# Kernel optimization log

Hardware: AMD Instinct MI355X
Metric: run time of the kernel (lower is better)

The kernel has to match this reference:

```python
import jax, jax.numpy as jnp
import numpy as np

N, IN_DIM, OUT_DIM, HEADS = 8192, 256, 128, 2


def setup_inputs() -> dict:
    key = jax.random.key(0)
    k1, k2, k3, k4, k5 = jax.random.split(key, 5)
    features = jax.random.normal(k1, (N, IN_DIM), dtype=jnp.float32)
    adjacency = jax.random.randint(k2, (N, N), 0, 2, dtype=jnp.int32)
    # nn.Linear(input_dim, output_dim*heads, bias=False): weight [out, in]
    W = jax.random.normal(k3, (OUT_DIM * HEADS, IN_DIM), dtype=jnp.float32) * 0.05
    attn_src = jax.random.normal(k4, (HEADS, OUT_DIM), dtype=jnp.float32) * 0.05
    attn_dst = jax.random.normal(k5, (HEADS, OUT_DIM), dtype=jnp.float32) * 0.05
    return {"features": features, "adjacency": adjacency, "W": W,
            "attn_src": attn_src, "attn_dst": attn_dst}


def reference(features, adjacency, W, attn_src, attn_dst):
    n = features.shape[0]
    # transformed: [N, H, F]
    transformed = (features @ W.T).reshape(n, HEADS, OUT_DIM)
    src_scores = jnp.einsum('nhf,hf->nh', transformed, attn_src)  # [N, H]
    dst_scores = jnp.einsum('nhf,hf->nh', transformed, attn_dst)  # [N, H]
    # logits: [N_src, N_dst, H]
    logits = jax.nn.leaky_relu(src_scores[:, None, :] + dst_scores[None, :, :],
                               negative_slope=0.2)
    mask = adjacency > 0  # [N, N]
    logits = jnp.where(mask[:, :, None], logits, -jnp.inf)
    attention = jax.nn.softmax(logits, axis=1)  # softmax over dst dim (dim=1)
    attention = jnp.nan_to_num(attention, nan=0.0, posinf=0.0, neginf=0.0)
    aggregated = jnp.einsum('ijh,jhf->ihf', attention, transformed)  # [N, H, F]
    return aggregated.mean(axis=1)  # [N, F]
```

## Files before the change

kernel.cpp:

```cpp
#include <hip/hip_runtime.h>
#include <stdint.h>
#include <stddef.h>

#define NN 8192
#define KD 256
#define CD 256
#define FD 128
#define BI 128
#define BJ 64
#define LOG2E 1.44269504f

typedef __attribute__((ext_vector_type(4))) float f32x4;
typedef __attribute__((ext_vector_type(2))) float f32x2;
typedef __attribute__((ext_vector_type(8))) short b16x8;

__device__ __forceinline__ unsigned int cvtpk(float lo, float hi) {
    unsigned int r;
    asm("v_cvt_pk_bf16_f32 %0, %1, %2" : "=v"(r) : "v"(lo), "v"(hi));
    return r;
}

__device__ __forceinline__ float exp2raw(float x) {
    float r;
    asm("v_exp_f32 %0, %1\n\ts_nop 0" : "=v"(r) : "v"(x));
    return r;
}

__device__ __forceinline__ void async16(const void* g, void* l) {
    __builtin_amdgcn_global_load_lds(
        (const __attribute__((address_space(1))) unsigned int*)g,
        (__attribute__((address_space(3))) unsigned int*)l, 16, 0, 0);
}

__global__ __launch_bounds__(256) void k_transform(
    const float* __restrict__ feat, const float* __restrict__ W,
    const float* __restrict__ asrc, const float* __restrict__ adst,
    unsigned short* __restrict__ Tt, float* __restrict__ s, float* __restrict__ d)
{
    __shared__ unsigned short a_lds[32 * 32];
    __shared__ unsigned short b_lds[256 * 32];
    __shared__ unsigned short tr_lds[256 * 40];
    __shared__ float sc_lds[4][32];
    __shared__ float dc_lds[4][32];

    const int t = threadIdx.x;
    const int wave = t >> 6, lane = t & 63;
    const int l15 = lane & 15, quad = lane >> 4;
    const int n0 = blockIdx.x * 32;

    f32x4 acc[2][4] = {};
    for (int kc = 0; kc < 8; ++kc) {
        const int k0 = kc * 32;
        __syncthreads();
        if (t < 128) {
            const int ai = t >> 2, ag = t & 3;
            const float* src = feat + (size_t)(n0 + ai) * KD + k0 + ag * 8;
            const float4 v0 = *(const float4*)src;
            const float4 v1 = *(const float4*)(src + 4);
            union { unsigned int u[4]; b16x8 v; } pk;
            pk.u[0] = cvtpk(v0.x, v0.y); pk.u[1] = cvtpk(v0.z, v0.w);
            pk.u[2] = cvtpk(v1.x, v1.y); pk.u[3] = cvtpk(v1.z, v1.w);
            const int slot = ag ^ ((ai >> 1) & 3);
            *(b16x8*)&a_lds[ai * 32 + slot * 8] = pk.v;
        }
        for (int p = 0; p < 4; ++p) {
            const int G = p * 256 + t;
            const int c = G >> 2, g = G & 3;
            const float* src = W + (size_t)c * KD + k0 + g * 8;
            const float4 v0 = *(const float4*)src;
            const float4 v1 = *(const float4*)(src + 4);
            union { unsigned int u[4]; b16x8 v; } pk;
            pk.u[0] = cvtpk(v0.x, v0.y); pk.u[1] = cvtpk(v0.z, v0.w);
            pk.u[2] = cvtpk(v1.x, v1.y); pk.u[3] = cvtpk(v1.z, v1.w);
            const int slot = g ^ ((c >> 1) & 3);
            *(b16x8*)&b_lds[c * 32 + slot * 8] = pk.v;
        }
        __syncthreads();
        b16x8 af[2], bfr[4];
        for (int mt = 0; mt < 2; ++mt) {
            const int m = mt * 16 + l15;
            af[mt] = *(const b16x8*)&a_lds[m * 32 + (quad ^ ((m >> 1) & 3)) * 8];
        }
        for (int nt = 0; nt < 4; ++nt) {
            const int c = wave * 64 + nt * 16 + l15;
            bfr[nt] = *(const b16x8*)&b_lds[c * 32 + (quad ^ ((c >> 1) & 3)) * 8];
        }
        for (int mt = 0; mt < 2; ++mt)
            for (int nt = 0; nt < 4; ++nt)
                acc[mt][nt] = __builtin_amdgcn_mfma_f32_16x16x32_bf16(
                    af[mt], bfr[nt], acc[mt][nt], 0, 0, 0);
    }

    float aS[4], aD[4];
    for (int nt = 0; nt < 4; ++nt) {
        const int c = wave * 64 + nt * 16 + l15;
        aS[nt] = asrc[c]; aD[nt] = adst[c];
    }
    for (int mt = 0; mt < 2; ++mt)
        for (int r = 0; r < 4; ++r) {
            float vs = 0.f, vd = 0.f;
            for (int nt = 0; nt < 4; ++nt) {
                const float x = acc[mt][nt][r];
                vs += x * aS[nt]; vd += x * aD[nt];
            }
            vs += __shfl_xor(vs, 1); vd += __shfl_xor(vd, 1);
            vs += __shfl_xor(vs, 2); vd += __shfl_xor(vd, 2);
            vs += __shfl_xor(vs, 4); vd += __shfl_xor(vd, 4);
            vs += __shfl_xor(vs, 8); vd += __shfl_xor(vd, 8);
            if (l15 == 0) {
                const int nl = mt * 16 + quad * 4 + r;
                sc_lds[wave][nl] = vs; dc_lds[wave][nl] = vd;
            }
        }
    for (int mt = 0; mt < 2; ++mt)
        for (int nt = 0; nt < 4; ++nt) {
            const int c = wave * 64 + nt * 16 + l15;
            const int n = mt * 16 + quad * 4;
            *(unsigned int*)&tr_lds[c * 40 + n] =
                cvtpk(acc[mt][nt][0], acc[mt][nt][1]);
            *(unsigned int*)&tr_lds[c * 40 + n + 2] =
                cvtpk(acc[mt][nt][2], acc[mt][nt][3]);
        }
    __syncthreads();
    if (t < 64) {
        const int n = t >> 1, h = t & 1;
        s[(size_t)(n0 + n) * 2 + h] = (sc_lds[h * 2][n] + sc_lds[h * 2 + 1][n]) * LOG2E;
        d[(size_t)(n0 + n) * 2 + h] = (dc_lds[h * 2][n] + dc_lds[h * 2 + 1][n]) * LOG2E;
    }
    for (int p = 0; p < 4; ++p) {
        const int idx = p * 256 + t;
        const int c = idx >> 2, g = idx & 3;
        *(b16x8*)(Tt + (size_t)c * NN + n0 + g * 8) = *(const b16x8*)&tr_lds[c * 40 + g * 8];
    }
}

__global__ __launch_bounds__(1024, 4) void k_gat(
    const int* __restrict__ adj, const unsigned short* __restrict__ Tt,
    const float* __restrict__ s, const float* __restrict__ d,
    float* __restrict__ num_part,
    float* __restrict__ den_part,
    int jchunk)
{
    __shared__ unsigned short tt_lds[2][CD * BJ];
    __shared__ unsigned short w_lds[2 * BI * BJ];

    const int t = threadIdx.x;
    const int w = t >> 6, lane = t & 63;
    const int l15 = lane & 15, quad = lane >> 4;
    const int rh = w & 3;
    const int cq = w >> 2;
    const int h  = cq >> 1;
    const int fh = cq & 1;
    const int i0 = blockIdx.x * BI;
    const int chunk = blockIdx.y;
    const int jbase = chunk * jchunk;

    const int wi = t >> 3;
    const int j8 = t & 7;
    const int gi = i0 + wi;
    const f32x2 s01 = *(const f32x2*)(s + (size_t)gi * 2);
    const int cbase = h * 128 + fh * 64;

    f32x4 acc[2][4] = {};
    float den0 = 0.f, den1 = 0.f;
    const int njt = jchunk / BJ;

    const int* arow = adj + (size_t)gi * NN + j8 * 8;
    const float* drow = d + (size_t)j8 * 16;
    const int c0 = w * 8 + (lane >> 3);
    const int g0 = (lane & 7) ^ (c0 & 7);
    const unsigned short* tsrc0 = Tt + (size_t)c0 * NN + g0 * 8;
    const int toff0 = w * 1024;
    const int slot = (j8 ^ (wi & 7)) << 3;
    unsigned short* wp0 = &w_lds[(0 * BI + wi) * BJ + slot];
    const int m0 = rh * 32 + l15;
    const int afb = (h * BI + m0) * BJ;
    const int bfb = (cbase + l15) * BJ;
    const int X[2] = {((0 * 4 + quad) ^ (l15 & 7)) << 3,
                      ((1 * 4 + quad) ^ (l15 & 7)) << 3};

    #pragma unroll
    for (int p = 0; p < 2; ++p)
        async16(tsrc0 + (size_t)p * 128 * NN + jbase,
                (char*)&tt_lds[0][0] + toff0 + p * 16384);
    int4 aA0 = *(const int4*)(arow + jbase);
    int4 aA1 = *(const int4*)(arow + jbase + 4);
    const float4* dpp = (const float4*)(drow + 2 * jbase);
    float4 dA0 = dpp[0], dA1 = dpp[1], dA2 = dpp[2], dA3 = dpp[3];
    int4 aB0, aB1; float4 dB0, dB1, dB2, dB3;

    auto body = [&](int jt, int buf,
                    int4& ca0, int4& ca1, float4& cd0, float4& cd1, float4& cd2, float4& cd3,
                    int4& na0, int4& na1, float4& nd0, float4& nd1, float4& nd2, float4& nd3) {
        const int j0 = jbase + jt * BJ;
        __builtin_amdgcn_s_barrier();
        const int jn = (jt + 1 < njt) ? j0 + BJ : j0;
        #pragma unroll
        for (int p = 0; p < 2; ++p)
            async16(tsrc0 + (size_t)p * 128 * NN + jn,
                    (char*)&tt_lds[buf ^ 1][0] + toff0 + p * 16384);
        na0 = *(const int4*)(arow + jn);
        na1 = *(const int4*)(arow + jn + 4);
        { const float4* dnp = (const float4*)(drow + 2 * jn);
          nd0 = dnp[0]; nd1 = dnp[1]; nd2 = dnp[2]; nd3 = dnp[3]; }
        union { float4 v[4]; f32x2 p[8]; } dv;
        dv.v[0] = cd0; dv.v[1] = cd1; dv.v[2] = cd2; dv.v[3] = cd3;
        const int am[8] = {ca0.x, ca0.y, ca0.z, ca0.w, ca1.x, ca1.y, ca1.z, ca1.w};
        f32x2 ef[8];
        f32x2 dp = {0.f, 0.f};
        #pragma unroll
        for (int e = 0; e < 8; ++e) {
            const f32x2 x = s01 + dv.p[e];
            const f32x2 xm = __builtin_elementwise_max(x, 0.2f * x);
            const float r0 = exp2raw(xm.x), r1 = exp2raw(xm.y);
            const f32x2 em = {am[e] != 0 ? r0 : 0.f, am[e] != 0 ? r1 : 0.f};
            ef[e] = em; dp += em;
        }
        den0 += dp.x; den1 += dp.y;
        union { unsigned int u[4]; b16x8 v; } w0, w1;
        #pragma unroll
        for (int q = 0; q < 4; ++q) {
            w0.u[q] = cvtpk(ef[2 * q].x, ef[2 * q + 1].x);
            w1.u[q] = cvtpk(ef[2 * q].y, ef[2 * q + 1].y);
        }
        *(b16x8*)wp0 = w0.v;
        *(b16x8*)(wp0 + BI * BJ) = w1.v;
        asm volatile("s_waitcnt vmcnt(8) lgkmcnt(0)" ::: "memory");
        __builtin_amdgcn_s_barrier();
        __builtin_amdgcn_sched_barrier(0);
        __builtin_amdgcn_s_setprio(1);
        #pragma unroll
        for (int ks = 0; ks < 2; ++ks) {
            b16x8 af[2], bf[4];
            #pragma unroll
            for (int mt = 0; mt < 2; ++mt)
                af[mt] = *(const b16x8*)&w_lds[afb + mt * 1024 + X[ks]];
            #pragma unroll
            for (int nt = 0; nt < 4; ++nt)
                bf[nt] = *(const b16x8*)&tt_lds[buf][bfb + nt * 1024 + X[ks]];
            #pragma unroll
            for (int mt = 0; mt < 2; ++mt)
                #pragma unroll
                for (int nt = 0; nt < 4; ++nt)
                    acc[mt][nt] = __builtin_amdgcn_mfma_f32_16x16x32_bf16(
                        af[mt], bf[nt], acc[mt][nt], 0, 0, 0);
        }
        __builtin_amdgcn_s_setprio(0);
    };

    for (int jt = 0; jt < njt; jt += 2) {
        body(jt,     0, aA0, aA1, dA0, dA1, dA2, dA3, aB0, aB1, dB0, dB1, dB2, dB3);
        body(jt + 1, 1, aB0, aB1, dB0, dB1, dB2, dB3, aA0, aA1, dA0, dA1, dA2, dA3);
    }
    asm volatile("s_waitcnt vmcnt(0)" ::: "memory");
    den0 += __shfl_xor(den0, 1); den0 += __shfl_xor(den0, 2); den0 += __shfl_xor(den0, 4);
    den1 += __shfl_xor(den1, 1); den1 += __shfl_xor(den1, 2); den1 += __shfl_xor(den1, 4);
    if (j8 == 0) {
        den_part[((size_t)chunk * 2 + 0) * NN + gi] = den0;
        den_part[((size_t)chunk * 2 + 1) * NN + gi] = den1;
    }
    float* np_ = num_part + (size_t)chunk * NN * CD;
    for (int mt = 0; mt < 2; ++mt)
        for (int nt = 0; nt < 4; ++nt)
            for (int r = 0; r < 4; ++r) {
                const int n = i0 + rh * 32 + mt * 16 + quad * 4 + r;
                const int c = cbase + nt * 16 + l15;
                np_[(size_t)n * CD + c] = acc[mt][nt][r];
            }
}

__global__ __launch_bounds__(256) void k_combine(
    const float* __restrict__ num_part, const float* __restrict__ den_part,
    float* __restrict__ out, int jsplit)
{
    const int idx = blockIdx.x * 256 + threadIdx.x;
    const int n = idx >> 7, f = idx & 127;
    const size_t row = (size_t)n * CD;
    float n0 = 0.f, n1 = 0.f, d0 = 0.f, d1 = 0.f;
    for (int c = 0; c < jsplit; ++c) {
        const size_t base = (size_t)c * NN * CD;
        n0 += num_part[base + row + f];
        n1 += num_part[base + row + 128 + f];
        d0 += den_part[((size_t)c * 2 + 0) * NN + n];
        d1 += den_part[((size_t)c * 2 + 1) * NN + n];
    }
    const float r0 = d0 != 0.f ? n0 / d0 : 0.f;
    const float r1 = d1 != 0.f ? n1 / d1 : 0.f;
    out[idx] = 0.5f * (r0 + r1);
}

extern "C" void kernel_launch(void* const* d_in, const int* in_sizes, int n_in,
                              void* d_out, int out_size, void* d_ws, size_t ws_size,
                              hipStream_t stream) {
    const float* feat = (const float*)d_in[0];
    const int*   adj  = (const int*)d_in[1];
    const float* W    = (const float*)d_in[2];
    const float* asrc = (const float*)d_in[3];
    const float* adst = (const float*)d_in[4];
    float* out = (float*)d_out;

    const int jsplit = (ws_size >= ((size_t)40 << 20)) ? 4 : 2;
    const int jchunk = NN / jsplit;

    char* ws = (char*)d_ws;
    unsigned short* Tt = (unsigned short*)ws;
    float* s    = (float*)(ws + ((size_t)4 << 20));
    float* dsc  = (float*)(ws + ((size_t)4 << 20) + (64 << 10));
    float* den  = (float*)(ws + ((size_t)4 << 20) + (128 << 10));
    float* nump = (float*)(ws + ((size_t)8 << 20));

    k_transform<<<256, 256, 0, stream>>>(feat, W, asrc, adst, Tt, s, dsc);
    k_gat<<<dim3(NN / BI, jsplit), 1024, 0, stream>>>(adj, Tt, s, dsc, nump, den, jchunk);
    k_combine<<<NN * FD / 256, 256, 0, stream>>>(nump, den, out, jsplit);
}
```

Before: 425.6 us.

## Pack adjacency into bitmask in transform kernel and compute weights in MFMA registers

Extra blocks in the fused transform kernel pack the int32 adjacency matrix into 64-bit ballot bitmasks. The attention kernel then reads bits instead of full ints and builds the exp weights directly in the MFMA A-operand registers, dropping the w_lds staging buffer and its LDS round trip. Each wave now covers 16 rows by 128 columns for one head, and jsplit grows to 4 or 8 depending on workspace size. The adjacency is still read once, but the bitmask pass is an added step, and the larger jsplit means more partial sums to write and combine.

```diff
diff --git a/kernel.cpp b/kernel.cpp
--- a/kernel.cpp
+++ b/kernel.cpp
@@ -32,10 +32,12 @@
         (__attribute__((address_space(3))) unsigned int*)l, 16, 0, 0);
 }
 
-__global__ __launch_bounds__(256) void k_transform(
+__global__ __launch_bounds__(256) void k_fused(
     const float* __restrict__ feat, const float* __restrict__ W,
     const float* __restrict__ asrc, const float* __restrict__ adst,
-    unsigned short* __restrict__ Tt, float* __restrict__ s, float* __restrict__ d)
+    const int* __restrict__ adj,
+    unsigned short* __restrict__ Tt, float* __restrict__ s, float* __restrict__ d,
+    unsigned long long* __restrict__ bits)
 {
     __shared__ unsigned short a_lds[32 * 32];
     __shared__ unsigned short b_lds[256 * 32];
@@ -44,6 +46,19 @@
     __shared__ float dc_lds[4][32];
 
     const int t = threadIdx.x;
+    if (blockIdx.x >= 256) {
+        const int lane = t & 63;
+        const int gw = (blockIdx.x - 256) * 4 + (t >> 6);
+        const int nwaves = (gridDim.x - 256) * 4;
+        const int total = NN * (NN / 64);
+        for (int idx = gw; idx < total; idx += nwaves) {
+            const int row = idx >> 7, w64 = idx & 127;
+            const int v = adj[(size_t)row * NN + w64 * 64 + lane];
+            const unsigned long long m = __ballot(v != 0);
+            if (lane == 0) bits[idx] = m;
+        }
+        return;
+    }
     const int wave = t >> 6, lane = t & 63;
     const int l15 = lane & 15, quad = lane >> 4;
     const int n0 = blockIdx.x * 32;
@@ -124,8 +139,8 @@
     __syncthreads();
     if (t < 64) {
         const int n = t >> 1, h = t & 1;
-        s[(size_t)(n0 + n) * 2 + h] = (sc_lds[h * 2][n] + sc_lds[h * 2 + 1][n]) * LOG2E;
-        d[(size_t)(n0 + n) * 2 + h] = (dc_lds[h * 2][n] + dc_lds[h * 2 + 1][n]) * LOG2E;
+        s[(size_t)h * NN + n0 + n] = (sc_lds[h * 2][n] + sc_lds[h * 2 + 1][n]) * LOG2E;
+        d[(size_t)h * NN + n0 + n] = (dc_lds[h * 2][n] + dc_lds[h * 2 + 1][n]) * LOG2E;
     }
     for (int p = 0; p < 4; ++p) {
         const int idx = p * 256 + t;
@@ -134,48 +149,38 @@
     }
 }
 
-__global__ __launch_bounds__(1024, 4) void k_gat(
-    const int* __restrict__ adj, const unsigned short* __restrict__ Tt,
+__global__ __launch_bounds__(1024, 8) void k_gat(
+    const unsigned long long* __restrict__ bits, const unsigned short* __restrict__ Tt,
     const float* __restrict__ s, const float* __restrict__ d,
     float* __restrict__ num_part,
     float* __restrict__ den_part,
     int jchunk)
 {
     __shared__ unsigned short tt_lds[2][CD * BJ];
-    __shared__ unsigned short w_lds[2 * BI * BJ];
 
     const int t = threadIdx.x;
     const int w = t >> 6, lane = t & 63;
     const int l15 = lane & 15, quad = lane >> 4;
-    const int rh = w & 3;
-    const int cq = w >> 2;
-    const int h  = cq >> 1;
-    const int fh = cq & 1;
+    const int rh = w & 7;
+    const int h  = w >> 3;
     const int i0 = blockIdx.x * BI;
     const int chunk = blockIdx.y;
     const int jbase = chunk * jchunk;
-
-    const int wi = t >> 3;
-    const int j8 = t & 7;
-    const int gi = i0 + wi;
-    const f32x2 s01 = *(const f32x2*)(s + (size_t)gi * 2);
-    const int cbase = h * 128 + fh * 64;
-
-    f32x4 acc[2][4] = {};
-    float den0 = 0.f, den1 = 0.f;
+    const int irow = i0 + rh * 16 + l15;
+    const float sr = s[(size_t)h * NN + irow];
     const int njt = jchunk / BJ;
 
-    const int* arow = adj + (size_t)gi * NN + j8 * 8;
-    const float* drow = d + (size_t)j8 * 16;
+    f32x4 acc[8] = {};
+    float den = 0.f;
+
     const int c0 = w * 8 + (lane >> 3);
     const int g0 = (lane & 7) ^ (c0 & 7);
     const unsigned short* tsrc0 = Tt + (size_t)c0 * NN + g0 * 8;
     const int toff0 = w * 1024;
-    const int slot = (j8 ^ (wi & 7)) << 3;
-    unsigned short* wp0 = &w_lds[(0 * BI + wi) * BJ + slot];
-    const int m0 = rh * 32 + l15;
-    const int afb = (h * BI + m0) * BJ;
-    const int bfb = (cbase + l15) * BJ;
+    const unsigned long long* brow = bits + (size_t)irow * (NN >> 6);
+    const int wb = jbase >> 6;
+    const float* drow = d + (size_t)h * NN + quad * 8;
+    const int bfb = (h * 128 + l15) * BJ;
     const int X[2] = {((0 * 4 + quad) ^ (l15 & 7)) << 3,
                       ((1 * 4 + quad) ^ (l15 & 7)) << 3};
 
@@ -183,90 +188,77 @@
     for (int p = 0; p < 2; ++p)
         async16(tsrc0 + (size_t)p * 128 * NN + jbase,
                 (char*)&tt_lds[0][0] + toff0 + p * 16384);
-    int4 aA0 = *(const int4*)(arow + jbase);
-    int4 aA1 = *(const int4*)(arow + jbase + 4);
-    const float4* dpp = (const float4*)(drow + 2 * jbase);
-    float4 dA0 = dpp[0], dA1 = dpp[1], dA2 = dpp[2], dA3 = dpp[3];
-    int4 aB0, aB1; float4 dB0, dB1, dB2, dB3;
-
-    auto body = [&](int jt, int buf,
-                    int4& ca0, int4& ca1, float4& cd0, float4& cd1, float4& cd2, float4& cd3,
-                    int4& na0, int4& na1, float4& nd0, float4& nd1, float4& nd2, float4& nd3) {
+
+    int buf = 0;
+    for (int jt = 0; jt < njt; ++jt) {
         const int j0 = jbase + jt * BJ;
         __builtin_amdgcn_s_barrier();
+        const unsigned long long cb = brow[wb + jt];
+        const float4 dv0 = *(const float4*)(drow + j0);
+        const float4 dv1 = *(const float4*)(drow + j0 + 4);
+        const float4 dv2 = *(const float4*)(drow + j0 + 32);
+        const float4 dv3 = *(const float4*)(drow + j0 + 36);
         const int jn = (jt + 1 < njt) ? j0 + BJ : j0;
         #pragma unroll
         for (int p = 0; p < 2; ++p)
             async16(tsrc0 + (size_t)p * 128 * NN + jn,
                     (char*)&tt_lds[buf ^ 1][0] + toff0 + p * 16384);
-        na0 = *(const int4*)(arow + jn);
-        na1 = *(const int4*)(arow + jn + 4);
-        { const float4* dnp = (const float4*)(drow + 2 * jn);
-          nd0 = dnp[0]; nd1 = dnp[1]; nd2 = dnp[2]; nd3 = dnp[3]; }
-        union { float4 v[4]; f32x2 p[8]; } dv;
-        dv.v[0] = cd0; dv.v[1] = cd1; dv.v[2] = cd2; dv.v[3] = cd3;
-        const int am[8] = {ca0.x, ca0.y, ca0.z, ca0.w, ca1.x, ca1.y, ca1.z, ca1.w};
-        f32x2 ef[8];
-        f32x2 dp = {0.f, 0.f};
-        #pragma unroll
-        for (int e = 0; e < 8; ++e) {
-            const f32x2 x = s01 + dv.p[e];
-            const f32x2 xm = __builtin_elementwise_max(x, 0.2f * x);
-            const float r0 = exp2raw(xm.x), r1 = exp2raw(xm.y);
-            const f32x2 em = {am[e] != 0 ? r0 : 0.f, am[e] != 0 ? r1 : 0.f};
-            ef[e] = em; dp += em;
-        }
-        den0 += dp.x; den1 += dp.y;
-        union { unsigned int u[4]; b16x8 v; } w0, w1;
-        #pragma unroll
-        for (int q = 0; q < 4; ++q) {
-            w0.u[q] = cvtpk(ef[2 * q].x, ef[2 * q + 1].x);
-            w1.u[q] = cvtpk(ef[2 * q].y, ef[2 * q + 1].y);
-        }
-        *(b16x8*)wp0 = w0.v;
-        *(b16x8*)(wp0 + BI * BJ) = w1.v;
-        asm volatile("s_waitcnt vmcnt(8) lgkmcnt(0)" ::: "memory");
+        const unsigned int by0 = (unsigned int)(cb >> (quad * 8)) & 0xffu;
+        const unsigned int by1 = (unsigned int)(cb >> (32 + quad * 8)) & 0xffu;
+        union { unsigned int u[4]; b16x8 v; } pa0, pa1;
+        {
+            const float dj[8] = {dv0.x, dv0.y, dv0.z, dv0.w, dv1.x, dv1.y, dv1.z, dv1.w};
+            float ef[8];
+            #pragma unroll
+            for (int e = 0; e < 8; ++e) {
+                float x = sr + dj[e]; x = fmaxf(x, 0.2f * x);
+                ef[e] = ((by0 >> e) & 1u) ? exp2raw(x) : 0.f;
+                den += ef[e];
+            }
+            #pragma unroll
+            for (int q = 0; q < 4; ++q) pa0.u[q] = cvtpk(ef[2 * q], ef[2 * q + 1]);
+        }
+        {
+            const float dj[8] = {dv2.x, dv2.y, dv2.z, dv2.w, dv3.x, dv3.y, dv3.z, dv3.w};
+            float ef[8];
+            #pragma unroll
+            for (int e = 0; e < 8; ++e) {
+                float x = sr + dj[e]; x = fmaxf(x, 0.2f * x);
+                ef[e] = ((by1 >> e) & 1u) ? exp2raw(x) : 0.f;
+                den += ef[e];
+            }
+            #pragma unroll
+            for (int q = 0; q < 4; ++q) pa1.u[q] = cvtpk(ef[2 * q], ef[2 * q + 1]);
+        }
+        asm volatile("s_waitcnt vmcnt(2)" ::: "memory");
         __builtin_amdgcn_s_barrier();
         __builtin_amdgcn_sched_barrier(0);
         __builtin_amdgcn_s_setprio(1);
         #pragma unroll
-        for (int ks = 0; ks < 2; ++ks) {
-            b16x8 af[2], bf[4];
-            #pragma unroll
-            for (int mt = 0; mt < 2; ++mt)
-                af[mt] = *(const b16x8*)&w_lds[afb + mt * 1024 + X[ks]];
-            #pragma unroll
-            for (int nt = 0; nt < 4; ++nt)
-                bf[nt] = *(const b16x8*)&tt_lds[buf][bfb + nt * 1024 + X[ks]];
-            #pragma unroll
-            for (int mt = 0; mt < 2; ++mt)
-                #pragma unroll
-                for (int nt = 0; nt < 4; ++nt)
-                    acc[mt][nt] = __builtin_amdgcn_mfma_f32_16x16x32_bf16(
-                        af[mt], bf[nt], acc[mt][nt], 0, 0, 0);
+        for (int nt = 0; nt < 8; ++nt) {
+            const b16x8 bf = *(const b16x8*)&tt_lds[buf][bfb + nt * 1024 + X[0]];
+            acc[nt] = __builtin_amdgcn_mfma_f32_16x16x32_bf16(pa0.v, bf, acc[nt], 0, 0, 0);
+        }
+        #pragma unroll
+        for (int nt = 0; nt < 8; ++nt) {
+            const b16x8 bf = *(const b16x8*)&tt_lds[buf][bfb + nt * 1024 + X[1]];
+            acc[nt] = __builtin_amdgcn_mfma_f32_16x16x32_bf16(pa1.v, bf, acc[nt], 0, 0, 0);
         }
         __builtin_amdgcn_s_setprio(0);
-    };
-
-    for (int jt = 0; jt < njt; jt += 2) {
-        body(jt,     0, aA0, aA1, dA0, dA1, dA2, dA3, aB0, aB1, dB0, dB1, dB2, dB3);
-        body(jt + 1, 1, aB0, aB1, dB0, dB1, dB2, dB3, aA0, aA1, dA0, dA1, dA2, dA3);
+        buf ^= 1;
     }
     asm volatile("s_waitcnt vmcnt(0)" ::: "memory");
-    den0 += __shfl_xor(den0, 1); den0 += __shfl_xor(den0, 2); den0 += __shfl_xor(den0, 4);
-    den1 += __shfl_xor(den1, 1); den1 += __shfl_xor(den1, 2); den1 += __shfl_xor(den1, 4);
-    if (j8 == 0) {
-        den_part[((size_t)chunk * 2 + 0) * NN + gi] = den0;
-        den_part[((size_t)chunk * 2 + 1) * NN + gi] = den1;
-    }
+    den += __shfl_xor(den, 16);
+    den += __shfl_xor(den, 32);
+    if (quad == 0)
+        den_part[((size_t)chunk * 2 + h) * NN + irow] = den;
     float* np_ = num_part + (size_t)chunk * NN * CD;
-    for (int mt = 0; mt < 2; ++mt)
-        for (int nt = 0; nt < 4; ++nt)
-            for (int r = 0; r < 4; ++r) {
-                const int n = i0 + rh * 32 + mt * 16 + quad * 4 + r;
-                const int c = cbase + nt * 16 + l15;
-                np_[(size_t)n * CD + c] = acc[mt][nt][r];
-            }
+    for (int nt = 0; nt < 8; ++nt)
+        for (int r = 0; r < 4; ++r) {
+            const int n = i0 + rh * 16 + quad * 4 + r;
+            const int c = h * 128 + nt * 16 + l15;
+            np_[(size_t)n * CD + c] = acc[nt][r];
+        }
 }
 
 __global__ __launch_bounds__(256) void k_combine(
@@ -299,7 +291,7 @@
     const float* adst = (const float*)d_in[4];
     float* out = (float*)d_out;
 
-    const int jsplit = (ws_size >= ((size_t)40 << 20)) ? 4 : 2;
+    const int jsplit = (ws_size >= ((size_t)81 << 20)) ? 8 : 4;
     const int jchunk = NN / jsplit;
 
     char* ws = (char*)d_ws;
@@ -308,8 +300,10 @@
     float* dsc  = (float*)(ws + ((size_t)4 << 20) + (64 << 10));
     float* den  = (float*)(ws + ((size_t)4 << 20) + (128 << 10));
     float* nump = (float*)(ws + ((size_t)8 << 20));
-
-    k_transform<<<256, 256, 0, stream>>>(feat, W, asrc, adst, Tt, s, dsc);
-    k_gat<<<dim3(NN / BI, jsplit), 1024, 0, stream>>>(adj, Tt, s, dsc, nump, den, jchunk);
+    unsigned long long* bits = (unsigned long long*)
+        (ws + ((size_t)(8 + 8 * (size_t)jsplit) << 20));
+
+    k_fused<<<2048, 256, 0, stream>>>(feat, W, asrc, adst, adj, Tt, s, dsc, bits);
+    k_gat<<<dim3(NN / BI, jsplit), 1024, 0, stream>>>(bits, Tt, s, dsc, nump, den, jchunk);
     k_combine<<<NN * FD / 256, 256, 0, stream>>>(nump, den, out, jsplit);
 }
```

After: 604.7 us. +42.1%, slower.
